# Kernel optimization log

Hardware: AMD Instinct MI355X
Metric: run time of the kernel (lower is better)

The kernel has to match this reference:

```python
import jax, jax.numpy as jnp
import numpy as np

NDIM = 4096      # ndim constructor arg; also hidden_node
BATCH = 2048
HID_F = 5        # hidden_feature (hardcoded in source)
STRIDE = 5       # encode_stride (hardcoded in source)


def _build_edges(ndim):
    # Faithful reproduction of the encoder edge construction in __init__.
    edges = []
    for j in range(ndim):
        c = j % ndim
        for i in range(c - STRIDE, c + STRIDE):
            edges.append([i % ndim, j])
    e = np.asarray(edges, dtype=np.int32).T  # [2, E], row=src, col=dst
    return e[0], e[1]


def setup_inputs() -> dict:
    key = jax.random.key(0)
    k1, k2, k3, k4, k5 = jax.random.split(key, 5)
    src, dst = _build_edges(NDIM)
    return {
        "x": jax.random.normal(k1, (BATCH, NDIM), jnp.float32),
        # PyG GraphConv((1, HID_F), HID_F): lin_rel Linear(1->HID_F, bias=True),
        # lin_root Linear(HID_F->HID_F, bias=False)
        "W_rel": jax.random.normal(k2, (HID_F, 1), jnp.float32) * 0.5,
        "b_rel": jax.random.normal(k3, (HID_F,), jnp.float32) * 0.1,
        "W_root": jax.random.normal(k4, (HID_F, HID_F), jnp.float32) * 0.1,
        # final Linear(ndim*HID_F -> ndim, bias=False)
        "W_final": jax.random.normal(k5, (NDIM, NDIM * HID_F), jnp.float32) * 0.01,
        "edge_src": jnp.asarray(src),
        "edge_dst": jnp.asarray(dst),
    }


def reference(x, W_rel, b_rel, W_root, W_final, edge_src, edge_dst):
    B, N = x.shape
    # gather source node features along edges: [B, E]
    vals = x[:, edge_src]
    # scatter-add into target nodes (sum aggregation): [B, N]
    agg = jax.ops.segment_sum(vals.T, edge_dst, num_segments=N).T
    # lin_rel (1 -> HID_F) applied to aggregated scalar feature
    z = agg[..., None] * W_rel[:, 0] + b_rel  # [B, N, HID_F]
    # lin_root applied to dst features z0 (zeros in this model) -- kept for faithfulness
    z0 = jnp.zeros((B, N, HID_F), x.dtype)
    z = z + z0 @ W_root.T
    z = jax.nn.relu(z)
    # final projection
    y = z.reshape(B, N * HID_F) @ W_final.T  # [B, N]
    return y
```

## Files before the change

### kernel.cpp

```cpp
#include <hip/hip_runtime.h>
#include <hip/hip_bf16.h>
#include <stdint.h>
#include <stddef.h>

#define NDIM  4096
#define BATCH 2048
#define HIDF  5
#define KDIM  (NDIM * HIDF)

typedef __bf16 bf16_t;
typedef __bf16 bf16x8 __attribute__((ext_vector_type(8)));
typedef float  f32x4  __attribute__((ext_vector_type(4)));

__device__ __forceinline__ void async_load_16B(const void* g, void* l) {
    __builtin_amdgcn_global_load_lds(
        (const __attribute__((address_space(1))) void*)g,
        (__attribute__((address_space(3))) void*)l,
        16, 0, 0);
}

__global__ void build_z(const float* __restrict__ x,
                        const float* __restrict__ W_rel,
                        const float* __restrict__ b_rel,
                        bf16_t* __restrict__ z)
{
    int idx = blockIdx.x * blockDim.x + threadIdx.x;
    int b = idx >> 12;
    int n = idx & (NDIM - 1);
    const float* xr = x + (size_t)b * NDIM;
    float agg = 0.f;
#pragma unroll
    for (int d = -5; d < 5; ++d)
        agg += xr[(n + d) & (NDIM - 1)];
    bf16_t* zr = z + (size_t)b * KDIM + n * HIDF;
#pragma unroll
    for (int f = 0; f < HIDF; ++f) {
        float v = fmaf(agg, W_rel[f], b_rel[f]);
        v = v > 0.f ? v : 0.f;
        zr[f] = (bf16_t)v;
    }
}

__global__ void cvt_w(const float* __restrict__ W, bf16_t* __restrict__ Wb,
                      int total8)
{
    int i = blockIdx.x * blockDim.x + threadIdx.x;
    int stride = gridDim.x * blockDim.x;
    for (; i < total8; i += stride) {
        const float* s = W + (size_t)i * 8;
        f32x4 v0 = *(const f32x4*)(s);
        f32x4 v1 = *(const f32x4*)(s + 4);
        bf16x8 pk;
        pk[0] = (bf16_t)v0[0]; pk[1] = (bf16_t)v0[1];
        pk[2] = (bf16_t)v0[2]; pk[3] = (bf16_t)v0[3];
        pk[4] = (bf16_t)v1[0]; pk[5] = (bf16_t)v1[1];
        pk[6] = (bf16_t)v1[2]; pk[7] = (bf16_t)v1[3];
        *(bf16x8*)(Wb + (size_t)i * 8) = pk;
    }
}

#define NT 160

__global__ __launch_bounds__(512, 2) void gemm8p(
    const bf16_t* __restrict__ Z,
    const bf16_t* __restrict__ Wb,
    float* __restrict__ Y,
    float* __restrict__ P)
{
    __shared__ char smem[131072];

    const int tid  = threadIdx.x;
    const int lane = tid & 63;
    const int wid  = tid >> 6;
    const int wr   = wid >> 2;
    const int wc   = wid & 3;

    const int bid   = blockIdx.x;
    const int split = bid & 1;
    const int tile  = bid >> 1;
    const int tm    = tile & 7;
    const int tn    = tile >> 3;
    const int m0    = tm * 256;
    const int n0    = tn * 256;
    const int kbase = split * (NT * 64);

    const int sr  = lane >> 3;
    const int scb = (lane & 7) ^ sr;
    const bf16_t* gA = Z  + (size_t)(m0 + wid * 8 + sr) * KDIM + kbase + scb * 8;
    const bf16_t* gB = Wb + (size_t)(n0 + wid * 8 + sr) * KDIM + kbase + scb * 8;

    const int r15  = lane & 15;
    const int xk   = (lane >> 4) << 4;
    const int xs   = (lane & 7) << 4;
    const int col0 = xk ^ xs;
    const int dcol = 64 - 2 * (col0 & 64);

    float* const out = split ? P : Y;

    f32x4 acc[8][4];
#pragma unroll
    for (int i = 0; i < 8; ++i)
#pragma unroll
        for (int j = 0; j < 4; ++j)
            acc[i][j] = (f32x4)0.f;

#pragma unroll
    for (int li = 0; li < 4; ++li) {
        async_load_16B(gA + (size_t)li * 64 * KDIM, smem + li * 8192 + wid * 1024);
        async_load_16B(gB + (size_t)li * 64 * KDIM, smem + 32768 + li * 8192 + wid * 1024);
    }

    for (int g = 0; g < NT; ++g) {
        char* const cb = smem + ((g & 1) ? 65536 : 0);
        char* const nb = smem + ((g & 1) ? 0 : 65536);
        const char* const pA = cb + (wr * 128 + r15) * 128 + col0;
        const char* const pB = cb + 32768 + (wc * 64 + r15) * 128 + col0;

        if (g + 1 < NT) {
            const bf16_t* const nA = gA + (size_t)(g + 1) * 64;
            const bf16_t* const nB = gB + (size_t)(g + 1) * 64;
#pragma unroll
            for (int li = 0; li < 4; ++li) {
                async_load_16B(nA + (size_t)li * 64 * KDIM, nb + li * 8192 + wid * 1024);
                async_load_16B(nB + (size_t)li * 64 * KDIM, nb + 32768 + li * 8192 + wid * 1024);
            }
            asm volatile("s_waitcnt vmcnt(8)" ::: "memory");
        } else {
            asm volatile("s_waitcnt vmcnt(0)" ::: "memory");
        }
        asm volatile("s_barrier" ::: "memory");

        bf16x8 a[8][2], b[4][2];
#pragma unroll
        for (int ni = 0; ni < 4; ++ni) {
            b[ni][0] = *(const bf16x8*)(pB + ni * 2048);
            b[ni][1] = *(const bf16x8*)(pB + ni * 2048 + dcol);
        }
#pragma unroll
        for (int mi = 0; mi < 8; ++mi) {
            a[mi][0] = *(const bf16x8*)(pA + mi * 2048);
            a[mi][1] = *(const bf16x8*)(pA + mi * 2048 + dcol);
        }
#pragma unroll
        for (int mi = 0; mi < 8; ++mi)
#pragma unroll
            for (int ni = 0; ni < 4; ++ni)
#pragma unroll
                for (int s = 0; s < 2; ++s)
                    acc[mi][ni] = __builtin_amdgcn_mfma_f32_16x16x32_bf16(
                        a[mi][s], b[ni][s], acc[mi][ni], 0, 0, 0);

        asm volatile("s_barrier" ::: "memory");
    }

    const int crow = m0 + wr * 128 + (lane >> 4) * 4;
    const int ccol = n0 + wc * 64 + (lane & 15);
#pragma unroll
    for (int mi = 0; mi < 8; ++mi)
#pragma unroll
        for (int ni = 0; ni < 4; ++ni) {
            float* cp = out + (size_t)(crow + mi * 16) * NDIM + ccol + ni * 16;
#pragma unroll
            for (int rr = 0; rr < 4; ++rr)
                cp[(size_t)rr * NDIM] = acc[mi][ni][rr];
        }
}

__global__ void add_y(float* __restrict__ y, const float* __restrict__ p, int n4)
{
    int i = blockIdx.x * blockDim.x + threadIdx.x;
    int st = gridDim.x * blockDim.x;
    for (; i < n4; i += st) {
        f32x4 a = ((const f32x4*)y)[i];
        f32x4 b = ((const f32x4*)p)[i];
        ((f32x4*)y)[i] = a + b;
    }
}

#define BM 128
#define BN 128
#define BK 64

__global__ __launch_bounds__(256) void gemm_bb(
    const bf16_t* __restrict__ Z,
    const bf16_t* __restrict__ Wb,
    float*        __restrict__ Y)
{
    __shared__ bf16_t As[BM * BK];
    __shared__ bf16_t Bs[BN * BK];

    const int tid  = threadIdx.x;
    const int lane = tid & 63;
    const int wid  = tid >> 6;
    const int bidm = blockIdx.x & 15;
    const int bidn = blockIdx.x >> 4;
    const int bm0 = bidm * BM;
    const int bn0 = bidn * BN;
    const int wr = wid >> 1, wc = wid & 1;

    f32x4 acc[4][4];
#pragma unroll
    for (int i = 0; i < 4; ++i)
#pragma unroll
        for (int j = 0; j < 4; ++j)
            acc[i][j] = (f32x4)0.f;

    const int arow_l = lane >> 3;
    const int acol_l = (lane & 7) * 8;

    for (int kt = 0; kt < KDIM / BK; ++kt) {
        const int k0 = kt * BK;
#pragma unroll
        for (int r = 0; r < 4; ++r) {
            const int chunk = wid * 4 + r;
            const int row   = chunk * 8 + arow_l;
            async_load_16B(Z + (size_t)(bm0 + row) * KDIM + k0 + acol_l,
                           (void*)(As + chunk * 512));
            async_load_16B(Wb + (size_t)(bn0 + row) * KDIM + k0 + acol_l,
                           (void*)(Bs + chunk * 512));
        }
        __syncthreads();
#pragma unroll
        for (int s = 0; s < 2; ++s) {
            bf16x8 af[4], bfr[4];
            const int ko = s * 32 + (lane >> 4) * 8;
#pragma unroll
            for (int mi = 0; mi < 4; ++mi)
                af[mi] = *(const bf16x8*)(As + (wr * 64 + mi * 16 + (lane & 15)) * BK + ko);
#pragma unroll
            for (int ni = 0; ni < 4; ++ni)
                bfr[ni] = *(const bf16x8*)(Bs + (wc * 64 + ni * 16 + (lane & 15)) * BK + ko);
#pragma unroll
            for (int mi = 0; mi < 4; ++mi)
#pragma unroll
                for (int ni = 0; ni < 4; ++ni)
                    acc[mi][ni] = __builtin_amdgcn_mfma_f32_16x16x32_bf16(
                        af[mi], bfr[ni], acc[mi][ni], 0, 0, 0);
        }
        __syncthreads();
    }

    const int crow = bm0 + wr * 64 + (lane >> 4) * 4;
    const int ccol = bn0 + wc * 64 + (lane & 15);
#pragma unroll
    for (int mi = 0; mi < 4; ++mi)
#pragma unroll
        for (int ni = 0; ni < 4; ++ni) {
            float* cp = Y + (size_t)(crow + mi * 16) * NDIM + ccol + ni * 16;
#pragma unroll
            for (int r = 0; r < 4; ++r)
                cp[(size_t)r * NDIM] = acc[mi][ni][r];
        }
}

__global__ __launch_bounds__(256) void gemm_zw(
    const bf16_t* __restrict__ Z,
    const float*  __restrict__ W,
    float*        __restrict__ Y)
{
    __shared__ bf16_t As[BM * BK];
    __shared__ bf16_t Bs[BN * BK];

    const int tid  = threadIdx.x;
    const int lane = tid & 63;
    const int wid  = tid >> 6;
    const int bidm = blockIdx.x & 15;
    const int bidn = blockIdx.x >> 4;
    const int bm0 = bidm * BM;
    const int bn0 = bidn * BN;
    const int wr = wid >> 1, wc = wid & 1;

    f32x4 acc[4][4];
#pragma unroll
    for (int i = 0; i < 4; ++i)
#pragma unroll
        for (int j = 0; j < 4; ++j)
            acc[i][j] = (f32x4)0.f;

    const int arow_l = lane >> 3;
    const int acol_l = (lane & 7) * 8;

    for (int kt = 0; kt < KDIM / BK; ++kt) {
        const int k0 = kt * BK;
#pragma unroll
        for (int r = 0; r < 4; ++r) {
            const int chunk = wid * 4 + r;
            const int row   = chunk * 8 + arow_l;
            async_load_16B(Z + (size_t)(bm0 + row) * KDIM + k0 + acol_l,
                           (void*)(As + chunk * 512));
        }
#pragma unroll
        for (int r = 0; r < 4; ++r) {
            const int chunk = wid * 4 + r;
            const int row   = chunk * 8 + arow_l;
            const float* src = W + (size_t)(bn0 + row) * KDIM + k0 + acol_l;
            f32x4 v0 = *(const f32x4*)(src);
            f32x4 v1 = *(const f32x4*)(src + 4);
            bf16x8 pk;
            pk[0] = (bf16_t)v0[0]; pk[1] = (bf16_t)v0[1];
            pk[2] = (bf16_t)v0[2]; pk[3] = (bf16_t)v0[3];
            pk[4] = (bf16_t)v1[0]; pk[5] = (bf16_t)v1[1];
            pk[6] = (bf16_t)v1[2]; pk[7] = (bf16_t)v1[3];
            *(bf16x8*)(Bs + chunk * 512 + lane * 8) = pk;
        }
        __syncthreads();
#pragma unroll
        for (int s = 0; s < 2; ++s) {
            bf16x8 af[4], bfr[4];
            const int ko = s * 32 + (lane >> 4) * 8;
#pragma unroll
            for (int mi = 0; mi < 4; ++mi)
                af[mi] = *(const bf16x8*)(As + (wr * 64 + mi * 16 + (lane & 15)) * BK + ko);
#pragma unroll
            for (int ni = 0; ni < 4; ++ni)
                bfr[ni] = *(const bf16x8*)(Bs + (wc * 64 + ni * 16 + (lane & 15)) * BK + ko);
#pragma unroll
            for (int mi = 0; mi < 4; ++mi)
#pragma unroll
                for (int ni = 0; ni < 4; ++ni)
                    acc[mi][ni] = __builtin_amdgcn_mfma_f32_16x16x32_bf16(
                        af[mi], bfr[ni], acc[mi][ni], 0, 0, 0);
        }
        __syncthreads();
    }

    const int crow = bm0 + wr * 64 + (lane >> 4) * 4;
    const int ccol = bn0 + wc * 64 + (lane & 15);
#pragma unroll
    for (int mi = 0; mi < 4; ++mi)
#pragma unroll
        for (int ni = 0; ni < 4; ++ni) {
            float* cp = Y + (size_t)(crow + mi * 16) * NDIM + ccol + ni * 16;
#pragma unroll
            for (int r = 0; r < 4; ++r)
                cp[(size_t)r * NDIM] = acc[mi][ni][r];
        }
}

extern "C" void kernel_launch(void* const* d_in, const int* in_sizes, int n_in,
                              void* d_out, int out_size, void* d_ws, size_t ws_size,
                              hipStream_t stream)
{
    const float* x      = (const float*)d_in[0];
    const float* W_rel  = (const float*)d_in[1];
    const float* b_rel  = (const float*)d_in[2];
    const float* W_fin  = (const float*)d_in[4];

    const size_t z_bytes  = (size_t)BATCH * KDIM * sizeof(bf16_t);
    const size_t wb_bytes = (size_t)NDIM  * KDIM * sizeof(bf16_t);
    const size_t p_bytes  = (size_t)BATCH * NDIM * sizeof(float);

    char* ws = (char*)d_ws;
    bf16_t* z  = (bf16_t*)ws;
    float*  y  = (float*)d_out;

    build_z<<<(BATCH * NDIM) / 256, 256, 0, stream>>>(x, W_rel, b_rel, z);

    if (ws_size >= z_bytes + wb_bytes + p_bytes) {
        bf16_t* Wb = (bf16_t*)(ws + z_bytes);
        float*  P  = (float*)(ws + z_bytes + wb_bytes);
        cvt_w<<<2048, 256, 0, stream>>>(W_fin, Wb, (int)((size_t)NDIM * KDIM / 8));
        gemm8p<<<256, 512, 0, stream>>>(z, Wb, y, P);
        add_y<<<2048, 256, 0, stream>>>(y, P, (BATCH * NDIM) / 4);
    } else if (ws_size >= z_bytes + wb_bytes) {
        bf16_t* Wb = (bf16_t*)(ws + z_bytes);
        cvt_w<<<2048, 256, 0, stream>>>(W_fin, Wb, (int)((size_t)NDIM * KDIM / 8));
        gemm_bb<<<(NDIM / BN) * (BATCH / BM), 256, 0, stream>>>(z, Wb, y);
    } else {
        gemm_zw<<<(NDIM / BN) * (BATCH / BM), 256, 0, stream>>>(z, W_fin, y);
    }
}
```

Baseline: 453.2 us.

## Switch GEMM to 32x32x16 MFMA with software-pipelined LDS reads

Replaces the 16x16x32 bf16 MFMA tiles with 32x32x16 tiles, which needs fewer LDS fragment reads per FLOP. The K-loop reads operands in four sub-steps with inline ds_read_b128 and explicit lgkmcnt waits, so LDS reads overlap the MFMAs. It also raises wave priority around the MFMA bursts. The epilogue is rewritten for the 32x32 accumulator layout, and the swizzled addressing must still match the layout the async loads write.

```diff
diff --git a/kernel.cpp b/kernel.cpp
--- a/kernel.cpp
+++ b/kernel.cpp
@@ -11,6 +11,7 @@
 typedef __bf16 bf16_t;
 typedef __bf16 bf16x8 __attribute__((ext_vector_type(8)));
 typedef float  f32x4  __attribute__((ext_vector_type(4)));
+typedef float  f32x16 __attribute__((ext_vector_type(16)));
 
 __device__ __forceinline__ void async_load_16B(const void* g, void* l) {
     __builtin_amdgcn_global_load_lds(
@@ -18,6 +19,9 @@
         (__attribute__((address_space(3))) void*)l,
         16, 0, 0);
 }
+
+#define DSR(dst, base, off) \
+    asm volatile("ds_read_b128 %0, %1 offset:" #off : "=v"(dst) : "v"(base))
 
 __global__ void build_z(const float* __restrict__ x,
                         const float* __restrict__ W_rel,
@@ -61,7 +65,7 @@
 
 #define NT 160
 
-__global__ __launch_bounds__(512, 2) void gemm8p(
+__global__ __launch_bounds__(512, 2) void gemm32(
     const bf16_t* __restrict__ Z,
     const bf16_t* __restrict__ Wb,
     float* __restrict__ Y,
@@ -89,20 +93,20 @@
     const bf16_t* gA = Z  + (size_t)(m0 + wid * 8 + sr) * KDIM + kbase + scb * 8;
     const bf16_t* gB = Wb + (size_t)(n0 + wid * 8 + sr) * KDIM + kbase + scb * 8;
 
-    const int r15  = lane & 15;
-    const int xk   = (lane >> 4) << 4;
-    const int xs   = (lane & 7) << 4;
-    const int col0 = xk ^ xs;
-    const int dcol = 64 - 2 * (col0 & 64);
+    const uint32_t l31 = lane & 31;
+    const uint32_t l7  = lane & 7;
+    const uint32_t hi  = lane >> 5;
+    const uint32_t rowA = (uint32_t)wr * 16384 + l31 * 128;
+    const uint32_t rowB = 32768u + (uint32_t)wc * 8192 + l31 * 128;
 
     float* const out = split ? P : Y;
 
-    f32x4 acc[8][4];
-#pragma unroll
-    for (int i = 0; i < 8; ++i)
-#pragma unroll
-        for (int j = 0; j < 4; ++j)
-            acc[i][j] = (f32x4)0.f;
+    f32x16 acc[4][2];
+#pragma unroll
+    for (int i = 0; i < 4; ++i)
+#pragma unroll
+        for (int j = 0; j < 2; ++j)
+            acc[i][j] = (f32x16)0.f;
 
 #pragma unroll
     for (int li = 0; li < 4; ++li) {
@@ -110,11 +114,36 @@
         async_load_16B(gB + (size_t)li * 64 * KDIM, smem + 32768 + li * 8192 + wid * 1024);
     }
 
+    bf16x8 aS0[4], bS0[2], aS1[4], bS1[2];
+
+#define READ6(AA, BB, S, CB)                                               \
+    {                                                                      \
+        uint32_t col = ((((uint32_t)(2 * (S)) + hi) ^ l7) << 4);           \
+        uint32_t adA = (CB) + rowA + col;                                  \
+        uint32_t adB = (CB) + rowB + col;                                  \
+        DSR(AA[0], adA, 0);     DSR(AA[1], adA, 4096);                     \
+        DSR(AA[2], adA, 8192);  DSR(AA[3], adA, 12288);                    \
+        DSR(BB[0], adB, 0);     DSR(BB[1], adB, 4096);                     \
+    }
+
+#define MFMA8(AA, BB)                                                      \
+    __builtin_amdgcn_s_setprio(1);                                         \
+    _Pragma("unroll")                                                      \
+    for (int fm = 0; fm < 4; ++fm) {                                       \
+        acc[fm][0] = __builtin_amdgcn_mfma_f32_32x32x16_bf16(              \
+            AA[fm], BB[0], acc[fm][0], 0, 0, 0);                           \
+        acc[fm][1] = __builtin_amdgcn_mfma_f32_32x32x16_bf16(              \
+            AA[fm], BB[1], acc[fm][1], 0, 0, 0);                           \
+    }                                                                      \
+    __builtin_amdgcn_s_setprio(0);
+
+#define WAITL(N)                                                           \
+    asm volatile("s_waitcnt lgkmcnt(" #N ")" ::: "memory");                \
+    __builtin_amdgcn_sched_barrier(0);
+
     for (int g = 0; g < NT; ++g) {
-        char* const cb = smem + ((g & 1) ? 65536 : 0);
+        const uint32_t cb = (g & 1) ? 65536u : 0u;
         char* const nb = smem + ((g & 1) ? 0 : 65536);
-        const char* const pA = cb + (wr * 128 + r15) * 128 + col0;
-        const char* const pB = cb + 32768 + (wc * 64 + r15) * 128 + col0;
 
         if (g + 1 < NT) {
             const bf16_t* const nA = gA + (size_t)(g + 1) * 64;
@@ -130,39 +159,35 @@
         }
         asm volatile("s_barrier" ::: "memory");
 
-        bf16x8 a[8][2], b[4][2];
-#pragma unroll
-        for (int ni = 0; ni < 4; ++ni) {
-            b[ni][0] = *(const bf16x8*)(pB + ni * 2048);
-            b[ni][1] = *(const bf16x8*)(pB + ni * 2048 + dcol);
-        }
-#pragma unroll
-        for (int mi = 0; mi < 8; ++mi) {
-            a[mi][0] = *(const bf16x8*)(pA + mi * 2048);
-            a[mi][1] = *(const bf16x8*)(pA + mi * 2048 + dcol);
-        }
-#pragma unroll
-        for (int mi = 0; mi < 8; ++mi)
-#pragma unroll
-            for (int ni = 0; ni < 4; ++ni)
-#pragma unroll
-                for (int s = 0; s < 2; ++s)
-                    acc[mi][ni] = __builtin_amdgcn_mfma_f32_16x16x32_bf16(
-                        a[mi][s], b[ni][s], acc[mi][ni], 0, 0, 0);
+        READ6(aS0, bS0, 0, cb)
+        READ6(aS1, bS1, 1, cb)
+        WAITL(6)
+        MFMA8(aS0, bS0)
+        READ6(aS0, bS0, 2, cb)
+        WAITL(6)
+        MFMA8(aS1, bS1)
+        READ6(aS1, bS1, 3, cb)
+        WAITL(6)
+        MFMA8(aS0, bS0)
+        WAITL(0)
+        MFMA8(aS1, bS1)
 
         asm volatile("s_barrier" ::: "memory");
     }
-
-    const int crow = m0 + wr * 128 + (lane >> 4) * 4;
-    const int ccol = n0 + wc * 64 + (lane & 15);
-#pragma unroll
-    for (int mi = 0; mi < 8; ++mi)
-#pragma unroll
-        for (int ni = 0; ni < 4; ++ni) {
-            float* cp = out + (size_t)(crow + mi * 16) * NDIM + ccol + ni * 16;
-#pragma unroll
-            for (int rr = 0; rr < 4; ++rr)
-                cp[(size_t)rr * NDIM] = acc[mi][ni][rr];
+#undef READ6
+#undef MFMA8
+#undef WAITL
+
+    const int ccol  = n0 + wc * 64 + (int)l31;
+    const int crow0 = m0 + wr * 128 + 4 * (int)hi;
+#pragma unroll
+    for (int fm = 0; fm < 4; ++fm)
+#pragma unroll
+        for (int fn = 0; fn < 2; ++fn) {
+            float* cp = out + (size_t)(crow0 + fm * 32) * NDIM + ccol + fn * 32;
+#pragma unroll
+            for (int r = 0; r < 16; ++r)
+                cp[(size_t)((r & 3) + 8 * (r >> 2)) * NDIM] = acc[fm][fn][r];
         }
 }
 
@@ -360,7 +385,7 @@
         bf16_t* Wb = (bf16_t*)(ws + z_bytes);
         float*  P  = (float*)(ws + z_bytes + wb_bytes);
         cvt_w<<<2048, 256, 0, stream>>>(W_fin, Wb, (int)((size_t)NDIM * KDIM / 8));
-        gemm8p<<<256, 512, 0, stream>>>(z, Wb, y, P);
+        gemm32<<<256, 512, 0, stream>>>(z, Wb, y, P);
         add_y<<<2048, 256, 0, stream>>>(y, P, (BATCH * NDIM) / 4);
     } else if (ws_size >= z_bytes + wb_bytes) {
         bf16_t* Wb = (bf16_t*)(ws + z_bytes);
```

New measurement: 480.4 us. 1.06x slower.

## Split gemm8p inner loop into four barrier-fenced MFMA quadrants with setprio

Applied to the files above, without the earlier changes.

Restructures the main GEMM's K-step into four phases that each load part of the A/B fragments from LDS and then run a quadrant of MFMAs under raised wave priority. Extra s_barriers between phases are meant to stagger waves so one wave's LDS reads overlap another wave's MFMA work, a ping-pong style schedule. Fragment registers drop from a[8] to a[4], which lowers register pressure. The cost is many more barriers per iteration, and the unused gemm_bb fallback path is removed.

```diff
diff --git a/kernel.cpp b/kernel.cpp
--- a/kernel.cpp
+++ b/kernel.cpp
@@ -110,11 +110,26 @@
         async_load_16B(gB + (size_t)li * 64 * KDIM, smem + 32768 + li * 8192 + wid * 1024);
     }
 
+#define MFMAQ(MBASE, N0)                                                   \
+    __builtin_amdgcn_s_setprio(1);                                         \
+    _Pragma("unroll")                                                      \
+    for (int s = 0; s < 2; ++s)                                            \
+        _Pragma("unroll")                                                  \
+        for (int mi = 0; mi < 4; ++mi)                                     \
+            _Pragma("unroll")                                              \
+            for (int ni = N0; ni < (N0) + 2; ++ni)                         \
+                acc[mi + (MBASE)][ni] =                                    \
+                    __builtin_amdgcn_mfma_f32_16x16x32_bf16(               \
+                        a[mi][s], b[ni][s], acc[mi + (MBASE)][ni], 0, 0, 0);\
+    __builtin_amdgcn_s_setprio(0);
+
     for (int g = 0; g < NT; ++g) {
         char* const cb = smem + ((g & 1) ? 65536 : 0);
         char* const nb = smem + ((g & 1) ? 0 : 65536);
         const char* const pA = cb + (wr * 128 + r15) * 128 + col0;
         const char* const pB = cb + 32768 + (wc * 64 + r15) * 128 + col0;
+
+        bf16x8 a[4][2], b[4][2];
 
         if (g + 1 < NT) {
             const bf16_t* const nA = gA + (size_t)(g + 1) * 64;
@@ -130,28 +145,49 @@
         }
         asm volatile("s_barrier" ::: "memory");
 
-        bf16x8 a[8][2], b[4][2];
-#pragma unroll
-        for (int ni = 0; ni < 4; ++ni) {
+#pragma unroll
+        for (int mi = 0; mi < 4; ++mi) {
+            a[mi][0] = *(const bf16x8*)(pA + mi * 2048);
+            a[mi][1] = *(const bf16x8*)(pA + mi * 2048 + dcol);
+        }
+#pragma unroll
+        for (int ni = 0; ni < 2; ++ni) {
             b[ni][0] = *(const bf16x8*)(pB + ni * 2048);
             b[ni][1] = *(const bf16x8*)(pB + ni * 2048 + dcol);
         }
-#pragma unroll
-        for (int mi = 0; mi < 8; ++mi) {
-            a[mi][0] = *(const bf16x8*)(pA + mi * 2048);
-            a[mi][1] = *(const bf16x8*)(pA + mi * 2048 + dcol);
-        }
-#pragma unroll
-        for (int mi = 0; mi < 8; ++mi)
-#pragma unroll
-            for (int ni = 0; ni < 4; ++ni)
-#pragma unroll
-                for (int s = 0; s < 2; ++s)
-                    acc[mi][ni] = __builtin_amdgcn_mfma_f32_16x16x32_bf16(
-                        a[mi][s], b[ni][s], acc[mi][ni], 0, 0, 0);
-
-        asm volatile("s_barrier" ::: "memory");
-    }
+        asm volatile("s_barrier" ::: "memory");
+        asm volatile("s_waitcnt lgkmcnt(0)" ::: "memory");
+        __builtin_amdgcn_sched_barrier(0);
+        MFMAQ(0, 0)
+        asm volatile("s_barrier" ::: "memory");
+
+#pragma unroll
+        for (int ni = 2; ni < 4; ++ni) {
+            b[ni][0] = *(const bf16x8*)(pB + ni * 2048);
+            b[ni][1] = *(const bf16x8*)(pB + ni * 2048 + dcol);
+        }
+        asm volatile("s_barrier" ::: "memory");
+        asm volatile("s_waitcnt lgkmcnt(0)" ::: "memory");
+        __builtin_amdgcn_sched_barrier(0);
+        MFMAQ(0, 2)
+        asm volatile("s_barrier" ::: "memory");
+
+#pragma unroll
+        for (int mi = 0; mi < 4; ++mi) {
+            a[mi][0] = *(const bf16x8*)(pA + (mi + 4) * 2048);
+            a[mi][1] = *(const bf16x8*)(pA + (mi + 4) * 2048 + dcol);
+        }
+        asm volatile("s_barrier" ::: "memory");
+        asm volatile("s_waitcnt lgkmcnt(0)" ::: "memory");
+        __builtin_amdgcn_sched_barrier(0);
+        MFMAQ(4, 0)
+        asm volatile("s_barrier" ::: "memory");
+
+        asm volatile("s_barrier" ::: "memory");
+        MFMAQ(4, 2)
+        asm volatile("s_barrier" ::: "memory");
+    }
+#undef MFMAQ
 
     const int crow = m0 + wr * 128 + (lane >> 4) * 4;
     const int ccol = n0 + wc * 64 + (lane & 15);
@@ -180,78 +216,6 @@
 #define BM 128
 #define BN 128
 #define BK 64
-
-__global__ __launch_bounds__(256) void gemm_bb(
-    const bf16_t* __restrict__ Z,
-    const bf16_t* __restrict__ Wb,
-    float*        __restrict__ Y)
-{
-    __shared__ bf16_t As[BM * BK];
-    __shared__ bf16_t Bs[BN * BK];
-
-    const int tid  = threadIdx.x;
-    const int lane = tid & 63;
-    const int wid  = tid >> 6;
-    const int bidm = blockIdx.x & 15;
-    const int bidn = blockIdx.x >> 4;
-    const int bm0 = bidm * BM;
-    const int bn0 = bidn * BN;
-    const int wr = wid >> 1, wc = wid & 1;
-
-    f32x4 acc[4][4];
-#pragma unroll
-    for (int i = 0; i < 4; ++i)
-#pragma unroll
-        for (int j = 0; j < 4; ++j)
-            acc[i][j] = (f32x4)0.f;
-
-    const int arow_l = lane >> 3;
-    const int acol_l = (lane & 7) * 8;
-
-    for (int kt = 0; kt < KDIM / BK; ++kt) {
-        const int k0 = kt * BK;
-#pragma unroll
-        for (int r = 0; r < 4; ++r) {
-            const int chunk = wid * 4 + r;
-            const int row   = chunk * 8 + arow_l;
-            async_load_16B(Z + (size_t)(bm0 + row) * KDIM + k0 + acol_l,
-                           (void*)(As + chunk * 512));
-            async_load_16B(Wb + (size_t)(bn0 + row) * KDIM + k0 + acol_l,
-                           (void*)(Bs + chunk * 512));
-        }
-        __syncthreads();
-#pragma unroll
-        for (int s = 0; s < 2; ++s) {
-            bf16x8 af[4], bfr[4];
-            const int ko = s * 32 + (lane >> 4) * 8;
-#pragma unroll
-            for (int mi = 0; mi < 4; ++mi)
-                af[mi] = *(const bf16x8*)(As + (wr * 64 + mi * 16 + (lane & 15)) * BK + ko);
-#pragma unroll
-            for (int ni = 0; ni < 4; ++ni)
-                bfr[ni] = *(const bf16x8*)(Bs + (wc * 64 + ni * 16 + (lane & 15)) * BK + ko);
-#pragma unroll
-            for (int mi = 0; mi < 4; ++mi)
-#pragma unroll
-                for (int ni = 0; ni < 4; ++ni)
-                    acc[mi][ni] = __builtin_amdgcn_mfma_f32_16x16x32_bf16(
-                        af[mi], bfr[ni], acc[mi][ni], 0, 0, 0);
-        }
-        __syncthreads();
-    }
-
-    const int crow = bm0 + wr * 64 + (lane >> 4) * 4;
-    const int ccol = bn0 + wc * 64 + (lane & 15);
-#pragma unroll
-    for (int mi = 0; mi < 4; ++mi)
-#pragma unroll
-        for (int ni = 0; ni < 4; ++ni) {
-            float* cp = Y + (size_t)(crow + mi * 16) * NDIM + ccol + ni * 16;
-#pragma unroll
-            for (int r = 0; r < 4; ++r)
-                cp[(size_t)r * NDIM] = acc[mi][ni][r];
-        }
-}
 
 __global__ __launch_bounds__(256) void gemm_zw(
     const bf16_t* __restrict__ Z,
@@ -362,10 +326,6 @@
         cvt_w<<<2048, 256, 0, stream>>>(W_fin, Wb, (int)((size_t)NDIM * KDIM / 8));
         gemm8p<<<256, 512, 0, stream>>>(z, Wb, y, P);
         add_y<<<2048, 256, 0, stream>>>(y, P, (BATCH * NDIM) / 4);
-    } else if (ws_size >= z_bytes + wb_bytes) {
-        bf16_t* Wb = (bf16_t*)(ws + z_bytes);
-        cvt_w<<<2048, 256, 0, stream>>>(W_fin, Wb, (int)((size_t)NDIM * KDIM / 8));
-        gemm_bb<<<(NDIM / BN) * (BATCH / BM), 256, 0, stream>>>(z, Wb, y);
     } else {
         gemm_zw<<<(NDIM / BN) * (BATCH / BM), 256, 0, stream>>>(z, W_fin, y);
     }
```

After: 487.4 us. 1.08x slower.
